# Optimization experiments

Hardware: AMD Instinct MI355X
Metric: run time of the kernel (lower is better)

## Reference

```python
import jax, jax.numpy as jnp
import numpy as np

D = 128  # dim_input / kernel_num
S = 1    # support_num
NL, NM, NG = 5, 20, 100

def _norm(x, axis):
    return x / jnp.maximum(jnp.linalg.norm(x, axis=axis, keepdims=True), 1e-12)

def _gather(t, idx):
    # t: (b,n,c), idx: (b,n,k) -> (b,n,k,c)
    return jax.vmap(lambda tb, ib: tb[ib])(t, idx)

def _knn(v, k):
    sq = jnp.sum(v * v, axis=-1)
    d = sq[:, :, None] + sq[:, None, :] - 2.0 * jnp.einsum('bic,bjc->bij', v, v)
    _, idx = jax.lax.top_k(-d, k + 1)
    return idx[:, :, 1:]  # drop self

def _conv_surface(idx, v, dirs):
    nd = _norm(_gather(v, idx) - v[:, :, None, :], -1)                    # (b,n,k,3)
    theta = jax.nn.relu(jnp.einsum('bnkc,cd->bnkd', nd, _norm(dirs, 0)))  # (b,n,k,S*D)
    b, n, k, _ = theta.shape
    theta = theta.reshape(b, n, k, S, D)
    return jnp.sum(jnp.max(theta, axis=2), axis=2)                         # (b,n,D)

def _conv_layer(idx, v, fm, W, bias, dirs):
    nd = _norm(_gather(v, idx) - v[:, :, None, :], -1)
    theta = jax.nn.relu(jnp.einsum('bnkc,cd->bnkd', nd, _norm(dirs, 0)))  # (b,n,k,S*D)
    fo = fm @ W + bias                                                    # (b,n,(S+1)*D)
    fc, fs = fo[..., :D], fo[..., D:]
    fs = _gather(fs, idx)                                                 # (b,n,k,S*D)
    b, n, k, _ = theta.shape
    act = (theta * fs).reshape(b, n, k, S, D)
    return fc + jnp.sum(jnp.max(act, axis=2), axis=2)                     # (b,n,D)

def _bn_relu(x, g, b, eps=1e-5):
    # training-mode BatchNorm1d over (batch, points) per channel, then ReLU
    m = jnp.mean(x, axis=(0, 1))
    v = jnp.var(x, axis=(0, 1))
    return jax.nn.relu((x - m) * jax.lax.rsqrt(v + eps) * g + b)

def setup_inputs() -> dict:
    key = jax.random.key(0)
    ks = jax.random.split(key, 16)
    B, N = 4, 1024
    def u(k, shape, fan):
        s = 1.0 / np.sqrt(fan)
        return jax.random.uniform(k, shape, jnp.float32, -s, s)
    inp = {}
    inp['vertices'] = jax.random.normal(ks[0], (B, N, 3), jnp.float32)
    inp['dirs_l'] = u(ks[1], (3, S * D), S * D)
    inp['dirs_m0'] = u(ks[2], (3, S * D), S * D)
    inp['W_m1'] = u(ks[3], (D, (S + 1) * D), (S + 1) * D)
    inp['b_m1'] = u(ks[4], ((S + 1) * D,), (S + 1) * D)
    inp['dirs_m1'] = u(ks[5], (3, S * D), S * D)
    inp['dirs_g0'] = u(ks[6], (3, S * D), S * D)
    inp['W_g1'] = u(ks[7], (D, (S + 1) * D), (S + 1) * D)
    inp['b_g1'] = u(ks[8], ((S + 1) * D,), (S + 1) * D)
    inp['dirs_g1'] = u(ks[9], (3, S * D), S * D)
    inp['W_g2'] = u(ks[10], (D, (S + 1) * D), (S + 1) * D)
    inp['b_g2'] = u(ks[11], ((S + 1) * D,), (S + 1) * D)
    inp['dirs_g2'] = u(ks[12], (3, S * D), S * D)
    for nm in ['l', 'm0', 'm1', 'g0', 'g1', 'g2']:
        inp['g_' + nm] = jnp.ones((D,), jnp.float32)
        inp['be_' + nm] = jnp.zeros((D,), jnp.float32)
    inp['W_down'] = u(ks[13], (3 * D, 2 * D), 3 * D)
    inp['b_down'] = u(ks[14], (2 * D,), 3 * D)
    return inp

def reference(vertices, dirs_l, dirs_m0, W_m1, b_m1, dirs_m1, dirs_g0, W_g1, b_g1, dirs_g1, W_g2, b_g2, dirs_g2, g_l, be_l, g_m0, be_m0, g_m1, be_m1, g_g0, be_g0, g_g1, be_g1, g_g2, be_g2, W_down, b_down):
    il = _knn(vertices, NL)
    im = _knn(vertices, NM)
    ig = _knn(vertices, NG)
    fm_l = _bn_relu(_conv_surface(il, vertices, dirs_l), g_l, be_l)
    fm_m = _bn_relu(_conv_surface(im, vertices, dirs_m0), g_m0, be_m0)
    fm_m = _bn_relu(_conv_layer(im, vertices, fm_m, W_m1, b_m1, dirs_m1), g_m1, be_m1)
    fm_g = _bn_relu(_conv_surface(ig, vertices, dirs_g0), g_g0, be_g0)
    fm_g = _bn_relu(_conv_layer(ig, vertices, fm_g, W_g1, b_g1, dirs_g1), g_g1, be_g1)
    fm_g = _bn_relu(_conv_layer(ig, vertices, fm_g, W_g2, b_g2, dirs_g2), g_g2, be_g2)
    out = jnp.concatenate((fm_l, fm_m, fm_g), axis=2)                      # (b,n,3D)
    return jax.nn.relu(out @ W_down + b_down)                              # (b,n,2D)
```

## Files before the change

kernel.cpp:

```cpp
#include <hip/hip_runtime.h>
#include <math.h>

typedef unsigned long long u64;

__global__ __launch_bounds__(256) void knnsurf_kernel(
    const float* __restrict__ verts,
    int* __restrict__ idx_out, float4* __restrict__ nd_out,
    const float* __restrict__ dl, const float* __restrict__ dm,
    const float* __restrict__ dg,
    float* __restrict__ raw_l, float* __restrict__ raw_m, float* __restrict__ raw_g)
{
    __shared__ float4 vps[1024];
    __shared__ __align__(16) u64 cand[4][208];
    const int tid = threadIdx.x;
    const int row0 = blockIdx.x * 4;
    const int b = row0 >> 10;
    const float* vb = verts + b * 3072;

    for (int n = tid; n < 1024; n += 256) {
        float x = vb[3 * n], y = vb[3 * n + 1], z = vb[3 * n + 2];
        float s = __fadd_rn(__fadd_rn(__fmul_rn(x, x), __fmul_rn(y, y)),
                            __fmul_rn(z, z));
        vps[n] = make_float4(x, y, z, s);
    }
    __syncthreads();

    const int w = tid >> 6, lane = tid & 63;
    const int row = row0 + w;
    const int n_i = row & 1023;
    const float4 pi = vps[n_i];
    const float xi = pi.x, yi = pi.y, zi = pi.z, sqi = pi.w;

    u64 K[16];
    u64 m1 = ~0ULL, m2 = ~0ULL;
#pragma unroll
    for (int t = 0; t < 16; ++t) {
        int j = t * 64 + lane;
        float4 p = vps[j];
        float dot = __fadd_rn(__fadd_rn(__fmul_rn(xi, p.x),
                                        __fmul_rn(yi, p.y)),
                              __fmul_rn(zi, p.z));
        float d = __fsub_rn(__fadd_rn(sqi, p.w), __fmul_rn(2.0f, dot));
        d = __fadd_rn(d, 0.0f);
        unsigned u = __float_as_uint(d);
        unsigned m = (u & 0x80000000u) ? ~u : (u | 0x80000000u);
        u64 k = ((u64)m << 10) | (unsigned)j;
        K[t] = k;
        bool lt1 = k < m1;
        u64 nm2 = lt1 ? m1 : ((k < m2) ? k : m2);
        m1 = lt1 ? k : m1;
        m2 = nm2;
    }

    u64 tmax = m2, tmin = m1;
#pragma unroll
    for (int off = 1; off < 64; off <<= 1) {
        u64 a = __shfl_xor(tmax, off); if (a > tmax) tmax = a;
        u64 c = __shfl_xor(tmin, off); if (c < tmin) tmin = c;
    }

    u64 T = tmax;
    int chi;
    {
        int c = 0;
#pragma unroll
        for (int t = 0; t < 16; ++t) c += (K[t] < T) ? 1 : 0;
#pragma unroll
        for (int off = 1; off < 64; off <<= 1) c += __shfl_xor(c, off);
        chi = c;
    }
    u64 lo = tmin, hi = T;
    while (chi > 192) {
        u64 mid = (lo + hi) >> 1;
        int c = 0;
#pragma unroll
        for (int t = 0; t < 16; ++t) c += (K[t] < mid) ? 1 : 0;
#pragma unroll
        for (int off = 1; off < 64; off <<= 1) c += __shfl_xor(c, off);
        if (c >= 101) { hi = mid; chi = c; } else lo = mid;
    }
    T = hi;
    const int n = chi;

    int myc_n = 0;
#pragma unroll
    for (int t = 0; t < 16; ++t) myc_n += (K[t] < T) ? 1 : 0;
    int sc = myc_n;
#pragma unroll
    for (int off = 1; off < 64; off <<= 1) {
        int v = __shfl_up(sc, off);
        if (lane >= off) sc += v;
    }
    int pos = sc - myc_n;
#pragma unroll
    for (int t = 0; t < 16; ++t) {
        if (K[t] < T) cand[w][pos++] = K[t];
    }
    if (lane == 0) cand[w][n] = ~0ULL;
    __syncthreads();

    u64 myc[3]; int rk[3];
#pragma unroll
    for (int q = 0; q < 3; ++q) {
        int i = lane + q * 64;
        myc[q] = (i < n) ? cand[w][i] : ~0ULL;
        rk[q] = 0;
    }
    {
        const ulonglong2* c2 = (const ulonglong2*)&cand[w][0];
        const int half = (n + 1) >> 1;
        for (int jj = 0; jj < half; ++jj) {
            ulonglong2 kk = c2[jj];
#pragma unroll
            for (int q = 0; q < 3; ++q) {
                rk[q] += (kk.x < myc[q]) ? 1 : 0;
                rk[q] += (kk.y < myc[q]) ? 1 : 0;
            }
        }
    }

    const int rowbase = row & ~1023;
    float4* nd4w = (float4*)&cand[w][0];
#pragma unroll
    for (int q = 0; q < 3; ++q) {
        int i = lane + q * 64;
        if (i < n) {
            int r = rk[q];
            if (r >= 1 && r <= 100) {
                int slot = r - 1;
                unsigned j = (unsigned)(myc[q] & 1023u);
                idx_out[row * 100 + slot] = rowbase + (int)j;
                float4 pj = vps[j];
                float dx = pj.x - xi, dy = pj.y - yi, dz = pj.z - zi;
                float nrm = sqrtf(__fadd_rn(__fadd_rn(__fmul_rn(dx, dx),
                                                      __fmul_rn(dy, dy)),
                                            __fmul_rn(dz, dz)));
                float inv = 1.0f / fmaxf(nrm, 1e-12f);
                float4 nv = make_float4(dx * inv, dy * inv, dz * inv, 0.0f);
                nd_out[row * 100 + slot] = nv;
                nd4w[slot] = nv;
            }
        }
    }
    __syncthreads();

    const int d = tid & 127;
    float lx = dl[d], ly = dl[128 + d], lz = dl[256 + d];
    float li = 1.0f / fmaxf(sqrtf((lx * lx + ly * ly) + lz * lz), 1e-12f);
    lx *= li; ly *= li; lz *= li;
    float mx = dm[d], my = dm[128 + d], mz = dm[256 + d];
    float mi = 1.0f / fmaxf(sqrtf((mx * mx + my * my) + mz * mz), 1e-12f);
    mx *= mi; my *= mi; mz *= mi;
    float gx = dg[d], gy = dg[128 + d], gz = dg[256 + d];
    float gi = 1.0f / fmaxf(sqrtf((gx * gx + gy * gy) + gz * gz), 1e-12f);
    gx *= gi; gy *= gi; gz *= gi;

#pragma unroll
    for (int p = 0; p < 2; ++p) {
        int rr = (tid >> 7) + 2 * p;
        const float4* ns = (const float4*)&cand[rr][0];
        float ml = -1e30f, mm = -1e30f, mg = -1e30f;
        int k = 0;
        for (; k < 5; ++k) {
            float4 v = ns[k];
            ml = fmaxf(ml, (v.x * lx + v.y * ly) + v.z * lz);
            mm = fmaxf(mm, (v.x * mx + v.y * my) + v.z * mz);
            mg = fmaxf(mg, (v.x * gx + v.y * gy) + v.z * gz);
        }
        for (; k < 20; ++k) {
            float4 v = ns[k];
            mm = fmaxf(mm, (v.x * mx + v.y * my) + v.z * mz);
            mg = fmaxf(mg, (v.x * gx + v.y * gy) + v.z * gz);
        }
        for (; k < 100; ++k) {
            float4 v = ns[k];
            mg = fmaxf(mg, (v.x * gx + v.y * gy) + v.z * gz);
        }
        int orow = row0 + rr;
        raw_l[orow * 128 + d] = fmaxf(ml, 0.0f);
        raw_m[orow * 128 + d] = fmaxf(mm, 0.0f);
        raw_g[orow * 128 + d] = fmaxf(mg, 0.0f);
    }
}

__global__ __launch_bounds__(256) void bnsum_kernel(
    const float* s0, double* p0,
    const float* s1, double* p1,
    const float* s2, double* p2)
{
    const int t = blockIdx.x >> 5;
    const int blk = blockIdx.x & 31;
    const float* src = (t == 0) ? s0 : (t == 1) ? s1 : s2;
    double* p = (t == 0) ? p0 : (t == 1) ? p1 : p2;
    const int tid = threadIdx.x;
    const int c = tid & 127, seg = tid >> 7;
    const float* q = src + ((size_t)blk * 128 + seg * 64) * 128 + c;
    double s = 0.0, ss = 0.0;
    for (int r = 0; r < 64; ++r) { float v = q[r * 128]; s += v; ss += (double)v * v; }
    __shared__ double Ls[2][128], Lq[2][128];
    Ls[seg][c] = s; Lq[seg][c] = ss;
    __syncthreads();
    if (tid < 128) {
        p[blk * 256 + c]       = Ls[0][c] + Ls[1][c];
        p[blk * 256 + 128 + c] = Lq[0][c] + Lq[1][c];
    }
}

__device__ __forceinline__ void compute_st(const double* __restrict__ p,
                                           const float* __restrict__ g,
                                           const float* __restrict__ e,
                                           float* stA, float* stB,
                                           int tid, int nthreads)
{
    for (int c = tid; c < 128; c += nthreads) {
        double S = 0.0, Q = 0.0;
#pragma unroll
        for (int bb = 0; bb < 32; ++bb) { S += p[bb * 256 + c]; Q += p[bb * 256 + 128 + c]; }
        double m = S * (1.0 / 4096.0);
        double var = Q * (1.0 / 4096.0) - m * m;
        double a = (double)g[c] / sqrt(var + 1e-5);
        stA[c] = (float)a;
        stB[c] = (float)((double)e[c] - m * a);
    }
}

__global__ __launch_bounds__(256) void gemm2_kernel(
    const float* __restrict__ Aa, const double* __restrict__ pa,
    const float* __restrict__ ga, const float* __restrict__ ea,
    const float* __restrict__ Wa, const float* __restrict__ ba, float* __restrict__ outa,
    const float* __restrict__ Ab, const double* __restrict__ pb,
    const float* __restrict__ gb, const float* __restrict__ eb,
    const float* __restrict__ Wb, const float* __restrict__ bb, float* __restrict__ outb)
{
    const int job = blockIdx.y;
    const float* A = job ? Ab : Aa;  const double* p = job ? pb : pa;
    const float* g = job ? gb : ga;  const float* e = job ? eb : ea;
    const float* W = job ? Wb : Wa;  const float* bias = job ? bb : ba;
    float* out = job ? outb : outa;

    __shared__ float stA[128], stB[128];
    __shared__ float As[8 * 128];
    const int o = threadIdx.x;
    const int r0 = blockIdx.x * 8;

    compute_st(p, g, e, stA, stB, o, 256);
    __syncthreads();

    for (int t = o; t < 8 * 128; t += 256) {
        int r = t >> 7, c = t & 127;
        As[t] = fmaxf(fmaf(stA[c], A[(r0 + r) * 128 + c], stB[c]), 0.0f);
    }
    __syncthreads();

    float acc[8];
    const float bz = bias[o];
#pragma unroll
    for (int r = 0; r < 8; ++r) acc[r] = bz;

    for (int c = 0; c < 128; c += 4) {
        float w0 = W[(c + 0) * 256 + o];
        float w1 = W[(c + 1) * 256 + o];
        float w2 = W[(c + 2) * 256 + o];
        float w3 = W[(c + 3) * 256 + o];
#pragma unroll
        for (int r = 0; r < 8; ++r) {
            const float4 av = *(const float4*)&As[r * 128 + c];
            acc[r] += av.x * w0 + av.y * w1 + av.z * w2 + av.w * w3;
        }
    }
#pragma unroll
    for (int r = 0; r < 8; ++r)
        out[(r0 + r) * 256 + o] = acc[r];
}

__global__ __launch_bounds__(128) void layer_kernel(
    const float4* __restrict__ nd, const int* __restrict__ idxbuf,
    const float* dir0, const float* fo0, float* out0, int K0,
    const float* dir1, const float* fo1, float* out1, int K1)
{
    const int job = blockIdx.y;
    const float* dirs = job ? dir1 : dir0;
    const float* fo = job ? fo1 : fo0;
    float* out = job ? out1 : out0;
    const int K = job ? K1 : K0;

    const int d = threadIdx.x;
    const int row = blockIdx.x;

    float dx = dirs[d], dy = dirs[128 + d], dz = dirs[256 + d];
    float di = 1.0f / fmaxf(sqrtf((dx * dx + dy * dy) + dz * dz), 1e-12f);
    dx *= di; dy *= di; dz *= di;

    const float4* ns = nd + (size_t)row * 100;
    const int* ib = idxbuf + (size_t)row * 100;

    float acc = -1e30f;
    for (int k = 0; k < K; ++k) {
        float4 v = ns[k];
        int ix = ib[k];
        float th = fmaxf((v.x * dx + v.y * dy) + v.z * dz, 0.0f);
        float fs = fo[ix * 256 + 128 + d];
        acc = fmaxf(acc, th * fs);
    }
    out[row * 128 + d] = fo[row * 256 + d] + acc;
}

__global__ __launch_bounds__(256) void gemmf_kernel(
    const float* __restrict__ A0, const double* __restrict__ p0,
    const float* __restrict__ g0, const float* __restrict__ e0,
    const float* __restrict__ A1, const double* __restrict__ p1,
    const float* __restrict__ g1, const float* __restrict__ e1,
    const float* __restrict__ A2, const double* __restrict__ p2,
    const float* __restrict__ g2, const float* __restrict__ e2,
    const float* __restrict__ W, const float* __restrict__ bias, float* __restrict__ out)
{
    __shared__ float stA[384], stB[384];
    __shared__ float As[8 * 384];
    const int o = threadIdx.x;
    const int r0 = blockIdx.x * 8;

    compute_st(p0, g0, e0, stA,       stB,       o, 256);
    compute_st(p1, g1, e1, stA + 128, stB + 128, o, 256);
    compute_st(p2, g2, e2, stA + 256, stB + 256, o, 256);
    __syncthreads();

    for (int t = o; t < 8 * 384; t += 256) {
        int r = t / 384, c = t - r * 384;
        int seg = c >> 7, cc = c & 127;
        const float* A = (seg == 0) ? A0 : (seg == 1) ? A1 : A2;
        As[t] = fmaxf(fmaf(stA[c], A[(r0 + r) * 128 + cc], stB[c]), 0.0f);
    }
    __syncthreads();

    float acc[8];
    const float bz = bias[o];
#pragma unroll
    for (int r = 0; r < 8; ++r) acc[r] = bz;

    for (int c = 0; c < 384; c += 4) {
        float w0 = W[(c + 0) * 256 + o];
        float w1 = W[(c + 1) * 256 + o];
        float w2 = W[(c + 2) * 256 + o];
        float w3 = W[(c + 3) * 256 + o];
#pragma unroll
        for (int r = 0; r < 8; ++r) {
            const float4 av = *(const float4*)&As[r * 384 + c];
            acc[r] += av.x * w0 + av.y * w1 + av.z * w2 + av.w * w3;
        }
    }
#pragma unroll
    for (int r = 0; r < 8; ++r)
        out[(r0 + r) * 256 + o] = fmaxf(acc[r], 0.0f);
}

extern "C" void kernel_launch(void* const* d_in, const int* in_sizes, int n_in,
                              void* d_out, int out_size, void* d_ws, size_t ws_size,
                              hipStream_t stream)
{
    (void)in_sizes; (void)n_in; (void)out_size; (void)ws_size;

    const float* verts   = (const float*)d_in[0];
    const float* dirs_l  = (const float*)d_in[1];
    const float* dirs_m0 = (const float*)d_in[2];
    const float* W_m1    = (const float*)d_in[3];
    const float* b_m1    = (const float*)d_in[4];
    const float* dirs_m1 = (const float*)d_in[5];
    const float* dirs_g0 = (const float*)d_in[6];
    const float* W_g1    = (const float*)d_in[7];
    const float* b_g1    = (const float*)d_in[8];
    const float* dirs_g1 = (const float*)d_in[9];
    const float* W_g2    = (const float*)d_in[10];
    const float* b_g2    = (const float*)d_in[11];
    const float* dirs_g2 = (const float*)d_in[12];
    const float* g_l  = (const float*)d_in[13]; const float* be_l  = (const float*)d_in[14];
    const float* g_m0 = (const float*)d_in[15]; const float* be_m0 = (const float*)d_in[16];
    const float* g_m1 = (const float*)d_in[17]; const float* be_m1 = (const float*)d_in[18];
    const float* g_g0 = (const float*)d_in[19]; const float* be_g0 = (const float*)d_in[20];
    const float* g_g1 = (const float*)d_in[21]; const float* be_g1 = (const float*)d_in[22];
    const float* g_g2 = (const float*)d_in[23]; const float* be_g2 = (const float*)d_in[24];
    const float* W_down = (const float*)d_in[25];
    const float* b_down = (const float*)d_in[26];

    char* ws = (char*)d_ws;
    const size_t MB = 1 << 20;
    int*    idx100 = (int*)   (ws + 0);
    double* p_l    = (double*)(ws + 0x1A0000);
    double* p_m0   = p_l  + 8192;
    double* p_m1   = p_m0 + 8192;
    double* p_g0   = p_m1 + 8192;
    double* p_g1   = p_g0 + 8192;
    double* p_g2   = p_g1 + 8192;
    float4* nd100  = (float4*)(ws + 2 * MB);
    float* raw_l  = (float*)(ws +  9 * MB);
    float* raw_m0 = (float*)(ws + 11 * MB);
    float* raw_g0 = (float*)(ws + 13 * MB);
    float* raw_m1 = (float*)(ws + 15 * MB);
    float* raw_g1 = (float*)(ws + 17 * MB);
    float* raw_g2 = (float*)(ws + 19 * MB);
    float* fo_m   = (float*)(ws + 21 * MB);
    float* fo_g   = (float*)(ws + 25 * MB);
    float* fo_g2  = (float*)(ws + 29 * MB);

    knnsurf_kernel<<<1024, 256, 0, stream>>>(verts, idx100, nd100,
                                             dirs_l, dirs_m0, dirs_g0,
                                             raw_l, raw_m0, raw_g0);
    bnsum_kernel<<<96, 256, 0, stream>>>(raw_l, p_l, raw_m0, p_m0, raw_g0, p_g0);
    gemm2_kernel<<<dim3(512, 2), 256, 0, stream>>>(
        raw_m0, p_m0, g_m0, be_m0, W_m1, b_m1, fo_m,
        raw_g0, p_g0, g_g0, be_g0, W_g1, b_g1, fo_g);
    layer_kernel<<<dim3(4096, 2), 128, 0, stream>>>(nd100, idx100,
                                                    dirs_m1, fo_m, raw_m1, 20,
                                                    dirs_g1, fo_g, raw_g1, 100);
    bnsum_kernel<<<64, 256, 0, stream>>>(raw_m1, p_m1, raw_g1, p_g1, raw_g1, p_g1);
    gemm2_kernel<<<dim3(512, 1), 256, 0, stream>>>(
        raw_g1, p_g1, g_g1, be_g1, W_g2, b_g2, fo_g2,
        raw_g1, p_g1, g_g1, be_g1, W_g2, b_g2, fo_g2);
    layer_kernel<<<dim3(4096, 1), 128, 0, stream>>>(nd100, idx100,
                                                    dirs_g2, fo_g2, raw_g2, 100,
                                                    dirs_g2, fo_g2, raw_g2, 100);
    bnsum_kernel<<<32, 256, 0, stream>>>(raw_g2, p_g2, raw_g2, p_g2, raw_g2, p_g2);
    gemmf_kernel<<<512, 256, 0, stream>>>(raw_l, p_l, g_l, be_l,
                                          raw_m1, p_m1, g_m1, be_m1,
                                          raw_g2, p_g2, g_g2, be_g2,
                                          W_down, b_down, (float*)d_out);
}
```

Baseline: 274.9 us.

## Split BN-apply into separate kernels and read normalized activations directly in GEMMs

Moves the BatchNorm scale/shift and ReLU out of the GEMM kernels into a dedicated bnapply kernel that writes normalized activations to workspace, including a concatenated 384-wide buffer for the final projection. The GEMMs no longer recompute per-channel statistics in every block (each block previously re-reduced 32 double partials per channel) and read A directly from global memory with 16-wide weight register blocking. This adds three kernel launches and an extra write/read pass over the activations, and the GEMMs now fetch A from global/L1 instead of LDS.

```diff
diff --git a/kernel.cpp b/kernel.cpp
--- a/kernel.cpp
+++ b/kernel.cpp
@@ -224,53 +224,77 @@
     }
 }
 
+__global__ __launch_bounds__(256) void bnapply_kernel(
+    const float* __restrict__ s0, const double* __restrict__ p0,
+    const float* __restrict__ g0, const float* __restrict__ e0,
+    float* __restrict__ d0, int str0, int off0,
+    const float* __restrict__ s1, const double* __restrict__ p1,
+    const float* __restrict__ g1, const float* __restrict__ e1,
+    float* __restrict__ d1, int str1, int off1,
+    const float* __restrict__ s2, const double* __restrict__ p2,
+    const float* __restrict__ g2, const float* __restrict__ e2,
+    float* __restrict__ d2, int str2, int off2)
+{
+    const int job = blockIdx.y;
+    const float* src = (job == 0) ? s0 : (job == 1) ? s1 : s2;
+    const double* p  = (job == 0) ? p0 : (job == 1) ? p1 : p2;
+    const float* g   = (job == 0) ? g0 : (job == 1) ? g1 : g2;
+    const float* e   = (job == 0) ? e0 : (job == 1) ? e1 : e2;
+    float* dst       = (job == 0) ? d0 : (job == 1) ? d1 : d2;
+    const int str    = (job == 0) ? str0 : (job == 1) ? str1 : str2;
+    const int off    = (job == 0) ? off0 : (job == 1) ? off1 : off2;
+
+    __shared__ float stA[128], stB[128];
+    const int tid = threadIdx.x;
+    compute_st(p, g, e, stA, stB, tid, 256);
+    __syncthreads();
+
+    const int r0 = blockIdx.x * 16;
+    for (int t = tid; t < 16 * 128; t += 256) {
+        int r = t >> 7, c = t & 127;
+        float v = src[(size_t)(r0 + r) * 128 + c];
+        dst[(size_t)(r0 + r) * str + off + c] =
+            fmaxf(fmaf(stA[c], v, stB[c]), 0.0f);
+    }
+}
+
 __global__ __launch_bounds__(256) void gemm2_kernel(
-    const float* __restrict__ Aa, const double* __restrict__ pa,
-    const float* __restrict__ ga, const float* __restrict__ ea,
-    const float* __restrict__ Wa, const float* __restrict__ ba, float* __restrict__ outa,
-    const float* __restrict__ Ab, const double* __restrict__ pb,
-    const float* __restrict__ gb, const float* __restrict__ eb,
-    const float* __restrict__ Wb, const float* __restrict__ bb, float* __restrict__ outb)
+    const float* __restrict__ Aa, const float* __restrict__ Wa,
+    const float* __restrict__ ba, float* __restrict__ outa,
+    const float* __restrict__ Ab, const float* __restrict__ Wb,
+    const float* __restrict__ bb, float* __restrict__ outb)
 {
     const int job = blockIdx.y;
-    const float* A = job ? Ab : Aa;  const double* p = job ? pb : pa;
-    const float* g = job ? gb : ga;  const float* e = job ? eb : ea;
-    const float* W = job ? Wb : Wa;  const float* bias = job ? bb : ba;
-    float* out = job ? outb : outa;
-
-    __shared__ float stA[128], stB[128];
-    __shared__ float As[8 * 128];
+    const float* __restrict__ A = job ? Ab : Aa;
+    const float* __restrict__ W = job ? Wb : Wa;
+    const float* __restrict__ bias = job ? bb : ba;
+    float* __restrict__ out = job ? outb : outa;
+
     const int o = threadIdx.x;
     const int r0 = blockIdx.x * 8;
-
-    compute_st(p, g, e, stA, stB, o, 256);
-    __syncthreads();
-
-    for (int t = o; t < 8 * 128; t += 256) {
-        int r = t >> 7, c = t & 127;
-        As[t] = fmaxf(fmaf(stA[c], A[(r0 + r) * 128 + c], stB[c]), 0.0f);
-    }
-    __syncthreads();
+    const float* Wp = W + o;
 
     float acc[8];
     const float bz = bias[o];
 #pragma unroll
     for (int r = 0; r < 8; ++r) acc[r] = bz;
 
-    for (int c = 0; c < 128; c += 4) {
-        float w0 = W[(c + 0) * 256 + o];
-        float w1 = W[(c + 1) * 256 + o];
-        float w2 = W[(c + 2) * 256 + o];
-        float w3 = W[(c + 3) * 256 + o];
-#pragma unroll
-        for (int r = 0; r < 8; ++r) {
-            const float4 av = *(const float4*)&As[r * 128 + c];
-            acc[r] += av.x * w0 + av.y * w1 + av.z * w2 + av.w * w3;
+    for (int c0 = 0; c0 < 128; c0 += 16) {
+        float w[16];
+#pragma unroll
+        for (int q = 0; q < 16; ++q) w[q] = Wp[(c0 + q) * 256];
+#pragma unroll
+        for (int cc = 0; cc < 16; cc += 4) {
+#pragma unroll
+            for (int r = 0; r < 8; ++r) {
+                const float4 a = *(const float4*)&A[(size_t)(r0 + r) * 128 + c0 + cc];
+                acc[r] += a.x * w[cc] + a.y * w[cc + 1] + a.z * w[cc + 2] + a.w * w[cc + 3];
+            }
         }
     }
 #pragma unroll
     for (int r = 0; r < 8; ++r)
-        out[(r0 + r) * 256 + o] = acc[r];
+        out[(size_t)(r0 + r) * 256 + o] = acc[r];
 }
 
 __global__ __launch_bounds__(128) void layer_kernel(
@@ -306,51 +330,35 @@
 }
 
 __global__ __launch_bounds__(256) void gemmf_kernel(
-    const float* __restrict__ A0, const double* __restrict__ p0,
-    const float* __restrict__ g0, const float* __restrict__ e0,
-    const float* __restrict__ A1, const double* __restrict__ p1,
-    const float* __restrict__ g1, const float* __restrict__ e1,
-    const float* __restrict__ A2, const double* __restrict__ p2,
-    const float* __restrict__ g2, const float* __restrict__ e2,
-    const float* __restrict__ W, const float* __restrict__ bias, float* __restrict__ out)
-{
-    __shared__ float stA[384], stB[384];
-    __shared__ float As[8 * 384];
+    const float* __restrict__ A,
+    const float* __restrict__ W, const float* __restrict__ bias,
+    float* __restrict__ out)
+{
     const int o = threadIdx.x;
     const int r0 = blockIdx.x * 8;
-
-    compute_st(p0, g0, e0, stA,       stB,       o, 256);
-    compute_st(p1, g1, e1, stA + 128, stB + 128, o, 256);
-    compute_st(p2, g2, e2, stA + 256, stB + 256, o, 256);
-    __syncthreads();
-
-    for (int t = o; t < 8 * 384; t += 256) {
-        int r = t / 384, c = t - r * 384;
-        int seg = c >> 7, cc = c & 127;
-        const float* A = (seg == 0) ? A0 : (seg == 1) ? A1 : A2;
-        As[t] = fmaxf(fmaf(stA[c], A[(r0 + r) * 128 + cc], stB[c]), 0.0f);
-    }
-    __syncthreads();
+    const float* Wp = W + o;
 
     float acc[8];
     const float bz = bias[o];
 #pragma unroll
     for (int r = 0; r < 8; ++r) acc[r] = bz;
 
-    for (int c = 0; c < 384; c += 4) {
-        float w0 = W[(c + 0) * 256 + o];
-        float w1 = W[(c + 1) * 256 + o];
-        float w2 = W[(c + 2) * 256 + o];
-        float w3 = W[(c + 3) * 256 + o];
-#pragma unroll
-        for (int r = 0; r < 8; ++r) {
-            const float4 av = *(const float4*)&As[r * 384 + c];
-            acc[r] += av.x * w0 + av.y * w1 + av.z * w2 + av.w * w3;
+    for (int c0 = 0; c0 < 384; c0 += 16) {
+        float w[16];
+#pragma unroll
+        for (int q = 0; q < 16; ++q) w[q] = Wp[(c0 + q) * 256];
+#pragma unroll
+        for (int cc = 0; cc < 16; cc += 4) {
+#pragma unroll
+            for (int r = 0; r < 8; ++r) {
+                const float4 a = *(const float4*)&A[(size_t)(r0 + r) * 384 + c0 + cc];
+                acc[r] += a.x * w[cc] + a.y * w[cc + 1] + a.z * w[cc + 2] + a.w * w[cc + 3];
+            }
         }
     }
 #pragma unroll
     for (int r = 0; r < 8; ++r)
-        out[(r0 + r) * 256 + o] = fmaxf(acc[r], 0.0f);
+        out[(size_t)(r0 + r) * 256 + o] = fmaxf(acc[r], 0.0f);
 }
 
 extern "C" void kernel_launch(void* const* d_in, const int* in_sizes, int n_in,
@@ -400,27 +408,40 @@
     float* fo_m   = (float*)(ws + 21 * MB);
     float* fo_g   = (float*)(ws + 25 * MB);
     float* fo_g2  = (float*)(ws + 29 * MB);
+    float* An_f   = (float*)(ws + 34 * MB);
+    float* An_m0  = (float*)(ws + 41 * MB);
+    float* An_g0  = (float*)(ws + 43 * MB);
+    float* An_g1  = (float*)(ws + 45 * MB);
 
     knnsurf_kernel<<<1024, 256, 0, stream>>>(verts, idx100, nd100,
                                              dirs_l, dirs_m0, dirs_g0,
                                              raw_l, raw_m0, raw_g0);
     bnsum_kernel<<<96, 256, 0, stream>>>(raw_l, p_l, raw_m0, p_m0, raw_g0, p_g0);
+    bnapply_kernel<<<dim3(256, 3), 256, 0, stream>>>(
+        raw_l,  p_l,  g_l,  be_l,  An_f,  384, 0,
+        raw_m0, p_m0, g_m0, be_m0, An_m0, 128, 0,
+        raw_g0, p_g0, g_g0, be_g0, An_g0, 128, 0);
     gemm2_kernel<<<dim3(512, 2), 256, 0, stream>>>(
-        raw_m0, p_m0, g_m0, be_m0, W_m1, b_m1, fo_m,
-        raw_g0, p_g0, g_g0, be_g0, W_g1, b_g1, fo_g);
+        An_m0, W_m1, b_m1, fo_m,
+        An_g0, W_g1, b_g1, fo_g);
     layer_kernel<<<dim3(4096, 2), 128, 0, stream>>>(nd100, idx100,
                                                     dirs_m1, fo_m, raw_m1, 20,
                                                     dirs_g1, fo_g, raw_g1, 100);
     bnsum_kernel<<<64, 256, 0, stream>>>(raw_m1, p_m1, raw_g1, p_g1, raw_g1, p_g1);
+    bnapply_kernel<<<dim3(256, 2), 256, 0, stream>>>(
+        raw_m1, p_m1, g_m1, be_m1, An_f,  384, 128,
+        raw_g1, p_g1, g_g1, be_g1, An_g1, 128, 0,
+        raw_g1, p_g1, g_g1, be_g1, An_g1, 128, 0);
     gemm2_kernel<<<dim3(512, 1), 256, 0, stream>>>(
-        raw_g1, p_g1, g_g1, be_g1, W_g2, b_g2, fo_g2,
-        raw_g1, p_g1, g_g1, be_g1, W_g2, b_g2, fo_g2);
+        An_g1, W_g2, b_g2, fo_g2,
+        An_g1, W_g2, b_g2, fo_g2);
     layer_kernel<<<dim3(4096, 1), 128, 0, stream>>>(nd100, idx100,
                                                     dirs_g2, fo_g2, raw_g2, 100,
                                                     dirs_g2, fo_g2, raw_g2, 100);
     bnsum_kernel<<<32, 256, 0, stream>>>(raw_g2, p_g2, raw_g2, p_g2, raw_g2, p_g2);
-    gemmf_kernel<<<512, 256, 0, stream>>>(raw_l, p_l, g_l, be_l,
-                                          raw_m1, p_m1, g_m1, be_m1,
-                                          raw_g2, p_g2, g_g2, be_g2,
-                                          W_down, b_down, (float*)d_out);
-}
+    bnapply_kernel<<<dim3(256, 1), 256, 0, stream>>>(
+        raw_g2, p_g2, g_g2, be_g2, An_f, 384, 256,
+        raw_g2, p_g2, g_g2, be_g2, An_f, 384, 256,
+        raw_g2, p_g2, g_g2, be_g2, An_f, 384, 256);
+    gemmf_kernel<<<512, 256, 0, stream>>>(An_f, W_down, b_down, (float*)d_out);
+}
```

Result: slower. 310.8 us (+13.0%).

## Retile GEMM kernels to 32-row by 64-column blocks with register-cached weights

Applied to the files above, without the earlier changes.

The two GEMM kernels (gemm2 and the final down-projection) now have each block handle 32 rows by 64 output columns instead of 8 rows by all 256 columns. Each of four thread groups computes 8 rows, and weights are loaded 16 at a time into registers so each weight read feeds 32 rows per block. The normalized input tile is staged with float4 loads. The aim is to cut redundant weight traffic per row and widen the global loads, at the cost of more shared memory (up to 48KB for gemmf) and more blocks redundantly recomputing the BN statistics.

```diff
diff --git a/kernel.cpp b/kernel.cpp
--- a/kernel.cpp
+++ b/kernel.cpp
@@ -232,45 +232,66 @@
     const float* __restrict__ gb, const float* __restrict__ eb,
     const float* __restrict__ Wb, const float* __restrict__ bb, float* __restrict__ outb)
 {
-    const int job = blockIdx.y;
-    const float* A = job ? Ab : Aa;  const double* p = job ? pb : pa;
-    const float* g = job ? gb : ga;  const float* e = job ? eb : ea;
-    const float* W = job ? Wb : Wa;  const float* bias = job ? bb : ba;
-    float* out = job ? outb : outa;
+    const int job = blockIdx.z;
+    const float* __restrict__ A = job ? Ab : Aa;
+    const double* __restrict__ p = job ? pb : pa;
+    const float* __restrict__ g = job ? gb : ga;
+    const float* __restrict__ e = job ? eb : ea;
+    const float* __restrict__ W = job ? Wb : Wa;
+    const float* __restrict__ bias = job ? bb : ba;
+    float* __restrict__ out = job ? outb : outa;
 
     __shared__ float stA[128], stB[128];
-    __shared__ float As[8 * 128];
-    const int o = threadIdx.x;
-    const int r0 = blockIdx.x * 8;
-
-    compute_st(p, g, e, stA, stB, o, 256);
-    __syncthreads();
-
-    for (int t = o; t < 8 * 128; t += 256) {
-        int r = t >> 7, c = t & 127;
-        As[t] = fmaxf(fmaf(stA[c], A[(r0 + r) * 128 + c], stB[c]), 0.0f);
-    }
-    __syncthreads();
+    __shared__ float As[32 * 128];
+    const int tid = threadIdx.x;
+    const int r0 = blockIdx.x * 32;
+
+    compute_st(p, g, e, stA, stB, tid, 256);
+    __syncthreads();
+
+    {
+        const float4* A4 = (const float4*)(A + (size_t)r0 * 128);
+        float4* As4 = (float4*)As;
+        for (int t = tid; t < 32 * 32; t += 256) {
+            int r = t >> 5, c4 = t & 31;
+            float4 v = A4[r * 32 + c4];
+            int c = c4 * 4;
+            float4 o4;
+            o4.x = fmaxf(fmaf(stA[c + 0], v.x, stB[c + 0]), 0.0f);
+            o4.y = fmaxf(fmaf(stA[c + 1], v.y, stB[c + 1]), 0.0f);
+            o4.z = fmaxf(fmaf(stA[c + 2], v.z, stB[c + 2]), 0.0f);
+            o4.w = fmaxf(fmaf(stA[c + 3], v.w, stB[c + 3]), 0.0f);
+            As4[t] = o4;
+        }
+    }
+    __syncthreads();
+
+    const int o = tid & 63;
+    const int h = tid >> 6;
+    const int gcol = blockIdx.y * 64 + o;
+    const float* Wp = W + gcol;
 
     float acc[8];
-    const float bz = bias[o];
+    const float bz = bias[gcol];
 #pragma unroll
     for (int r = 0; r < 8; ++r) acc[r] = bz;
 
-    for (int c = 0; c < 128; c += 4) {
-        float w0 = W[(c + 0) * 256 + o];
-        float w1 = W[(c + 1) * 256 + o];
-        float w2 = W[(c + 2) * 256 + o];
-        float w3 = W[(c + 3) * 256 + o];
-#pragma unroll
-        for (int r = 0; r < 8; ++r) {
-            const float4 av = *(const float4*)&As[r * 128 + c];
-            acc[r] += av.x * w0 + av.y * w1 + av.z * w2 + av.w * w3;
+    for (int c0 = 0; c0 < 128; c0 += 16) {
+        float w[16];
+#pragma unroll
+        for (int q = 0; q < 16; ++q) w[q] = Wp[(c0 + q) * 256];
+#pragma unroll
+        for (int cc = 0; cc < 16; cc += 4) {
+#pragma unroll
+            for (int r = 0; r < 8; ++r) {
+                const float4 a = *(const float4*)&As[(h * 8 + r) * 128 + c0 + cc];
+                acc[r] += a.x * w[cc] + a.y * w[cc + 1] + a.z * w[cc + 2] + a.w * w[cc + 3];
+            }
         }
     }
 #pragma unroll
     for (int r = 0; r < 8; ++r)
-        out[(r0 + r) * 256 + o] = acc[r];
+        out[(size_t)(r0 + h * 8 + r) * 256 + gcol] = acc[r];
 }
 
 __global__ __launch_bounds__(128) void layer_kernel(
@@ -315,42 +336,59 @@
     const float* __restrict__ W, const float* __restrict__ bias, float* __restrict__ out)
 {
     __shared__ float stA[384], stB[384];
-    __shared__ float As[8 * 384];
-    const int o = threadIdx.x;
-    const int r0 = blockIdx.x * 8;
-
-    compute_st(p0, g0, e0, stA,       stB,       o, 256);
-    compute_st(p1, g1, e1, stA + 128, stB + 128, o, 256);
-    compute_st(p2, g2, e2, stA + 256, stB + 256, o, 256);
-    __syncthreads();
-
-    for (int t = o; t < 8 * 384; t += 256) {
-        int r = t / 384, c = t - r * 384;
-        int seg = c >> 7, cc = c & 127;
-        const float* A = (seg == 0) ? A0 : (seg == 1) ? A1 : A2;
-        As[t] = fmaxf(fmaf(stA[c], A[(r0 + r) * 128 + cc], stB[c]), 0.0f);
-    }
-    __syncthreads();
+    __shared__ float As[32 * 384];
+    const int tid = threadIdx.x;
+    const int r0 = blockIdx.x * 32;
+
+    compute_st(p0, g0, e0, stA,       stB,       tid, 256);
+    compute_st(p1, g1, e1, stA + 128, stB + 128, tid, 256);
+    compute_st(p2, g2, e2, stA + 256, stB + 256, tid, 256);
+    __syncthreads();
+
+    {
+        float4* As4 = (float4*)As;
+        for (int t = tid; t < 32 * 96; t += 256) {
+            int r = t / 96, c4 = t - r * 96;
+            int seg = c4 >> 5, cc4 = c4 & 31;
+            const float* A = (seg == 0) ? A0 : (seg == 1) ? A1 : A2;
+            float4 v = *(const float4*)&A[((size_t)(r0 + r) * 32 + cc4) * 4];
+            int c = c4 * 4;
+            float4 o4;
+            o4.x = fmaxf(fmaf(stA[c + 0], v.x, stB[c + 0]), 0.0f);
+            o4.y = fmaxf(fmaf(stA[c + 1], v.y, stB[c + 1]), 0.0f);
+            o4.z = fmaxf(fmaf(stA[c + 2], v.z, stB[c + 2]), 0.0f);
+            o4.w = fmaxf(fmaf(stA[c + 3], v.w, stB[c + 3]), 0.0f);
+            As4[t] = o4;
+        }
+    }
+    __syncthreads();
+
+    const int o = tid & 63;
+    const int h = tid >> 6;
+    const int gcol = blockIdx.y * 64 + o;
+    const float* Wp = W + gcol;
 
     float acc[8];
-    const float bz = bias[o];
+    const float bz = bias[gcol];
 #pragma unroll
     for (int r = 0; r < 8; ++r) acc[r] = bz;
 
-    for (int c = 0; c < 384; c += 4) {
-        float w0 = W[(c + 0) * 256 + o];
-        float w1 = W[(c + 1) * 256 + o];
-        float w2 = W[(c + 2) * 256 + o];
-        float w3 = W[(c + 3) * 256 + o];
-#pragma unroll
-        for (int r = 0; r < 8; ++r) {
-            const float4 av = *(const float4*)&As[r * 384 + c];
-            acc[r] += av.x * w0 + av.y * w1 + av.z * w2 + av.w * w3;
+    for (int c0 = 0; c0 < 384; c0 += 16) {
+        float w[16];
+#pragma unroll
+        for (int q = 0; q < 16; ++q) w[q] = Wp[(c0 + q) * 256];
+#pragma unroll
+        for (int cc = 0; cc < 16; cc += 4) {
+#pragma unroll
+            for (int r = 0; r < 8; ++r) {
+                const float4 a = *(const float4*)&As[(h * 8 + r) * 384 + c0 + cc];
+                acc[r] += a.x * w[cc] + a.y * w[cc + 1] + a.z * w[cc + 2] + a.w * w[cc + 3];
+            }
         }
     }
 #pragma unroll
     for (int r = 0; r < 8; ++r)
-        out[(r0 + r) * 256 + o] = fmaxf(acc[r], 0.0f);
+        out[(size_t)(r0 + h * 8 + r) * 256 + gcol] = fmaxf(acc[r], 0.0f);
 }
 
 extern "C" void kernel_launch(void* const* d_in, const int* in_sizes, int n_in,
@@ -405,22 +443,22 @@
                                              dirs_l, dirs_m0, dirs_g0,
                                              raw_l, raw_m0, raw_g0);
     bnsum_kernel<<<96, 256, 0, stream>>>(raw_l, p_l, raw_m0, p_m0, raw_g0, p_g0);
-    gemm2_kernel<<<dim3(512, 2), 256, 0, stream>>>(
+    gemm2_kernel<<<dim3(128, 4, 2), 256, 0, stream>>>(
         raw_m0, p_m0, g_m0, be_m0, W_m1, b_m1, fo_m,
         raw_g0, p_g0, g_g0, be_g0, W_g1, b_g1, fo_g);
     layer_kernel<<<dim3(4096, 2), 128, 0, stream>>>(nd100, idx100,
                                                     dirs_m1, fo_m, raw_m1, 20,
                                                     dirs_g1, fo_g, raw_g1, 100);
     bnsum_kernel<<<64, 256, 0, stream>>>(raw_m1, p_m1, raw_g1, p_g1, raw_g1, p_g1);
-    gemm2_kernel<<<dim3(512, 1), 256, 0, stream>>>(
+    gemm2_kernel<<<dim3(128, 4, 1), 256, 0, stream>>>(
         raw_g1, p_g1, g_g1, be_g1, W_g2, b_g2, fo_g2,
         raw_g1, p_g1, g_g1, be_g1, W_g2, b_g2, fo_g2);
     layer_kernel<<<dim3(4096, 1), 128, 0, stream>>>(nd100, idx100,
                                                     dirs_g2, fo_g2, raw_g2, 100,
                                                     dirs_g2, fo_g2, raw_g2, 100);
     bnsum_kernel<<<32, 256, 0, stream>>>(raw_g2, p_g2, raw_g2, p_g2, raw_g2, p_g2);
-    gemmf_kernel<<<512, 256, 0, stream>>>(raw_l, p_l, g_l, be_l,
-                                          raw_m1, p_m1, g_m1, be_m1,
-                                          raw_g2, p_g2, g_g2, be_g2,
-                                          W_down, b_down, (float*)d_out);
-}
+    gemmf_kernel<<<dim3(128, 4), 256, 0, stream>>>(raw_l, p_l, g_l, be_l,
+                                                   raw_m1, p_m1, g_m1, be_m1,
+                                                   raw_g2, p_g2, g_g2, be_g2,
+                                                   W_down, b_down, (float*)d_out);
+}
```

Measured after the change: 290.8 us. 5.8% more time.
